# Kernel optimization log

Hardware: AMD Instinct MI355X
Metric: run time of the kernel (lower is better)

## Reference

```python
import jax, jax.numpy as jnp
import numpy as np

B, C, H, W = 16, 512, 64, 64
R = 8
CP = C // R  # inner channel dim C' = 64


def setup_inputs() -> dict:
    key = jax.random.key(0)
    ks = jax.random.split(key, 10)
    s_in = 1.0 / np.sqrt(C)
    s_cp = 1.0 / np.sqrt(CP)
    return {
        "x": jax.random.normal(ks[0], (B, C, H, W), dtype=jnp.float32),
        "wq": jax.random.uniform(ks[1], (CP, C), jnp.float32, -s_in, s_in),
        "bq": jax.random.uniform(ks[2], (CP,), jnp.float32, -s_in, s_in),
        "wk": jax.random.uniform(ks[3], (CP, C), jnp.float32, -s_in, s_in),
        "bk": jax.random.uniform(ks[4], (CP,), jnp.float32, -s_in, s_in),
        "wv": jax.random.uniform(ks[5], (CP, C), jnp.float32, -s_in, s_in),
        "bv": jax.random.uniform(ks[6], (CP,), jnp.float32, -s_in, s_in),
        "wo": jax.random.uniform(ks[7], (C, CP), jnp.float32, -s_cp, s_cp),
        "bo": jax.random.uniform(ks[8], (C,), jnp.float32, -s_cp, s_cp),
        # torch init is gamma=0 (output==x, zero grads to convs); use small
        # nonzero value so the reference exercises the full graph.
        "gamma": jax.random.normal(ks[9], (1,), dtype=jnp.float32) * 0.1,
    }


def reference(x, wq, bq, wk, bk, wv, bv, wo, bo, gamma):
    b, c, h, w = x.shape
    n = h * w
    xf = x.reshape(b, c, n)  # flatten spatial -> (B, C, N)
    # 1x1 convs == channel matmuls
    q = jnp.einsum("oc,bcn->bon", wq, xf) + bq[:, None]  # (B, C', N)
    k = jnp.einsum("oc,bcn->bon", wk, xf) + bk[:, None]  # (B, C', N)
    v = jnp.einsum("oc,bcn->bon", wv, xf) + bv[:, None]  # (B, C', N)
    # energy = bmm(key (B,C',N), query^T (B,N,C')) -> (B, C', C')
    energy = jnp.einsum("bin,bjn->bij", k, q)
    attention = jax.nn.softmax(energy, axis=-1)  # (B, C', C')
    out = jnp.einsum("bij,bjn->bin", attention, v)  # (B, C', N)
    out = jnp.einsum("co,bon->bcn", wo, out) + bo[:, None]  # (B, C, N)
    out = out.reshape(b, c, h, w)
    return gamma * out + x
```

## Files before the change

### kernel.cpp

```cpp
#include <hip/hip_runtime.h>


#define NN 4096
#define CIN 512
#define CPD 64

typedef short s8v __attribute__((ext_vector_type(8)));
typedef float f4v __attribute__((ext_vector_type(4)));
typedef unsigned short u16;

__device__ __forceinline__ u16 f2bf(float f) {
    union { float f; unsigned int u; } c; c.f = f;
    unsigned int r = c.u + 0x7FFFu + ((c.u >> 16) & 1u);
    return (u16)(r >> 16);
}

__global__ __launch_bounds__(256) void k_prep(
    const float* __restrict__ wq, const float* __restrict__ wk,
    const float* __restrict__ wv, const float* __restrict__ wo,
    u16* __restrict__ wqkvb, u16* __restrict__ wob)
{
    const int t = blockIdx.x * 256 + threadIdx.x;
    const int i4 = t * 4;
    const float* src; u16* dst; int off;
    if (i4 < 98304) {
        const int r = i4 >> 15;
        src = (r == 0) ? wq : (r == 1) ? wk : wv;
        off = i4 & 32767;
        dst = wqkvb + (r << 15);
    } else {
        src = wo; off = i4 - 98304; dst = wob;
    }
    float4 v = *(const float4*)(src + off);
    u16 tmp[4] = { f2bf(v.x), f2bf(v.y), f2bf(v.z), f2bf(v.w) };
    *(uint2*)(dst + off) = *(const uint2*)tmp;
}

__global__ __launch_bounds__(256) void k_xt(
    const float* __restrict__ x, u16* __restrict__ xt)
{
    const int ct = blockIdx.x, nt = blockIdx.y, b = blockIdx.z;
    const int t = threadIdx.x;
    const int c0 = ct * 64, n0 = nt * 64;
    __shared__ u16 lt[64 * 64];

    #pragma unroll
    for (int p = 0; p < 4; ++p) {
        const int c_l = p * 16 + (t >> 4);
        const int n4  = (t & 15) * 4;
        float4 v = *(const float4*)(x + ((size_t)b * CIN + c0 + c_l) * NN + n0 + n4);
        u16 tmp[4] = { f2bf(v.x), f2bf(v.y), f2bf(v.z), f2bf(v.w) };
        *(uint2*)&lt[c_l * 64 + (n4 ^ ((c_l >> 3) << 3))] = *(const uint2*)tmp;
    }
    __syncthreads();

    #pragma unroll
    for (int pp = 0; pp < 2; ++pp) {
        const int n_l = pp * 32 + (t >> 3);
        const int cg  = (t & 7) * 8;
        const int swz = (t & 7) << 3;
        u16 tmp[8];
        #pragma unroll
        for (int i = 0; i < 8; ++i)
            tmp[i] = lt[(cg + i) * 64 + (n_l ^ swz)];
        *(uint4*)(xt + ((size_t)b * NN + n0 + n_l) * CIN + c0 + cg) =
            *(const uint4*)tmp;
    }
}

__global__ __launch_bounds__(256, 4) void k_qkv(
    const u16* __restrict__ xt, const u16* __restrict__ wqkvb,
    const float* __restrict__ bq, const float* __restrict__ bk,
    const float* __restrict__ bv,
    u16* __restrict__ q, u16* __restrict__ k, u16* __restrict__ vt)
{
    const int nb = blockIdx.x, b = blockIdx.y;
    const int t = threadIdx.x;
    const int w = t >> 6, L = t & 63, quad = L >> 4, l15 = L & 15;
    const int n0 = nb * 64;

    f4v acc[3][4];
    #pragma unroll
    for (int p = 0; p < 3; ++p)
        #pragma unroll
        for (int nn = 0; nn < 4; ++nn) acc[p][nn] = (f4v){0.f,0.f,0.f,0.f};

    const u16* xb = xt + ((size_t)b * NN + n0) * CIN;
    const u16* wb = wqkvb + (size_t)(w * 16 + l15) * CIN;

    #pragma unroll
    for (int ks = 0; ks < 16; ++ks) {
        const int c = ks * 32 + quad * 8;
        s8v bf[4], af[3];
        #pragma unroll
        for (int nn = 0; nn < 4; ++nn)
            bf[nn] = *(const s8v*)(xb + (size_t)(nn * 16 + l15) * CIN + c);
        #pragma unroll
        for (int p = 0; p < 3; ++p)
            af[p] = *(const s8v*)(wb + (size_t)p * 64 * CIN + c);
        #pragma unroll
        for (int p = 0; p < 3; ++p)
            #pragma unroll
            for (int nn = 0; nn < 4; ++nn)
                acc[p][nn] = __builtin_amdgcn_mfma_f32_16x16x32_bf16(
                    af[p], bf[nn], acc[p][nn], 0, 0, 0);
    }

    const int orow = w * 16 + quad * 4;
    {
        float4 q4 = *(const float4*)(bq + orow);
        float4 k4 = *(const float4*)(bk + orow);
        const float qb_[4] = { q4.x, q4.y, q4.z, q4.w };
        const float kb_[4] = { k4.x, k4.y, k4.z, k4.w };
        u16* qp = q + (size_t)b * CPD * NN;
        u16* kp = k + (size_t)b * CPD * NN;
        #pragma unroll
        for (int nn = 0; nn < 4; ++nn) {
            const int n = n0 + nn * 16 + l15;
            #pragma unroll
            for (int r = 0; r < 4; ++r) {
                qp[(size_t)(orow + r) * NN + n] = f2bf(acc[0][nn][r] + qb_[r]);
                kp[(size_t)(orow + r) * NN + n] = f2bf(acc[1][nn][r] + kb_[r]);
            }
        }
    }
    {
        float4 v4 = *(const float4*)(bv + orow);
        const float vb_[4] = { v4.x, v4.y, v4.z, v4.w };
        u16* vtb = vt + (size_t)b * NN * CPD;
        #pragma unroll
        for (int nn = 0; nn < 4; ++nn) {
            const int n = n0 + nn * 16 + l15;
            u16 tmp[4];
            #pragma unroll
            for (int r = 0; r < 4; ++r) tmp[r] = f2bf(acc[2][nn][r] + vb_[r]);
            *(uint2*)(vtb + (size_t)n * CPD + orow) = *(const uint2*)tmp;
        }
    }
}

__global__ __launch_bounds__(256, 4) void k_energy(
    const u16* __restrict__ q, const u16* __restrict__ k,
    float* __restrict__ epart)
{
    const int s = blockIdx.x;
    const int b = blockIdx.y;
    const int t = threadIdx.x;
    const int wv_ = t >> 6, L = t & 63, quad = L >> 4, l15 = L & 15;
    const u16* kb = k + (size_t)b * CPD * NN;
    const u16* qb = q + (size_t)b * CPD * NN;

    f4v acc[4][4];
    #pragma unroll
    for (int a = 0; a < 4; ++a)
        #pragma unroll
        for (int d = 0; d < 4; ++d) acc[a][d] = (f4v){0.f,0.f,0.f,0.f};

    const int nbase = s * 512 + wv_ * 128;
    #pragma unroll
    for (int ksl = 0; ksl < 4; ++ksl) {
        const int n = nbase + ksl * 32 + quad * 8;
        s8v af[4], bf_[4];
        #pragma unroll
        for (int it = 0; it < 4; ++it)
            af[it] = *(const s8v*)(kb + (size_t)(it * 16 + l15) * NN + n);
        #pragma unroll
        for (int jt = 0; jt < 4; ++jt)
            bf_[jt] = *(const s8v*)(qb + (size_t)(jt * 16 + l15) * NN + n);
        #pragma unroll
        for (int it = 0; it < 4; ++it)
            #pragma unroll
            for (int jt = 0; jt < 4; ++jt)
                acc[it][jt] = __builtin_amdgcn_mfma_f32_16x16x32_bf16(
                    af[it], bf_[jt], acc[it][jt], 0, 0, 0);
    }

    float* ep = epart + ((size_t)b * 32 + s * 4 + wv_) * 4096;
    #pragma unroll
    for (int it = 0; it < 4; ++it)
        #pragma unroll
        for (int jt = 0; jt < 4; ++jt)
            #pragma unroll
            for (int r = 0; r < 4; ++r)
                ep[(it * 16 + quad * 4 + r) * 64 + jt * 16 + l15] =
                    acc[it][jt][r];
}

__global__ __launch_bounds__(64) void k_softmax(
    const float* __restrict__ epart, u16* __restrict__ attn)
{
    const int i = blockIdx.x;
    const int b = blockIdx.y;
    const int j = threadIdx.x;
    float s = 0.f;
    #pragma unroll
    for (int sp = 0; sp < 32; ++sp)
        s += epart[((size_t)b * 32 + sp) * 4096 + i * 64 + j];
    float m = s;
    #pragma unroll
    for (int off = 32; off; off >>= 1) m = fmaxf(m, __shfl_xor(m, off));
    float e = __expf(s - m);
    float tot = e;
    #pragma unroll
    for (int off = 32; off; off >>= 1) tot += __shfl_xor(tot, off);
    attn[(size_t)b * 4096 + i * 64 + j] = f2bf(e / tot);
}

__global__ __launch_bounds__(256, 4) void k_avout(
    const u16* __restrict__ vt, const u16* __restrict__ attn,
    const u16* __restrict__ wob, const float* __restrict__ bo,
    const float* __restrict__ gamma, const float* __restrict__ x,
    float* __restrict__ out)
{
    const int nb = blockIdx.x, b = blockIdx.y;
    const int t = threadIdx.x;
    const int wv_ = t >> 6, L = t & 63, quad = L >> 4, l15 = L & 15;
    const int swz = (l15 & 7) * 8;

    __shared__ u16 avl[128 * 64];

    {
        const u16* ab  = attn + (size_t)b * 4096;
        const u16* vtb = vt + (size_t)b * NN * CPD;
        const int n0 = nb * 128;
        f4v acc1[4][2];
        #pragma unroll
        for (int a = 0; a < 4; ++a)
            #pragma unroll
            for (int d = 0; d < 2; ++d) acc1[a][d] = (f4v){0.f,0.f,0.f,0.f};
        #pragma unroll
        for (int ks = 0; ks < 2; ++ks) {
            const int j = ks * 32 + quad * 8;
            s8v af[4], bf_[2];
            #pragma unroll
            for (int it = 0; it < 4; ++it)
                af[it] = *(const s8v*)(ab + (size_t)(it * 16 + l15) * 64 + j);
            #pragma unroll
            for (int nn = 0; nn < 2; ++nn)
                bf_[nn] = *(const s8v*)(vtb +
                    (size_t)(n0 + wv_ * 32 + nn * 16 + l15) * CPD + j);
            #pragma unroll
            for (int it = 0; it < 4; ++it)
                #pragma unroll
                for (int nn = 0; nn < 2; ++nn)
                    acc1[it][nn] = __builtin_amdgcn_mfma_f32_16x16x32_bf16(
                        af[it], bf_[nn], acc1[it][nn], 0, 0, 0);
        }
        #pragma unroll
        for (int it = 0; it < 4; ++it)
            #pragma unroll
            for (int nn = 0; nn < 2; ++nn) {
                const int nloc = wv_ * 32 + nn * 16 + l15;
                u16 tmp[4];
                #pragma unroll
                for (int r = 0; r < 4; ++r) tmp[r] = f2bf(acc1[it][nn][r]);
                *(uint2*)&avl[nloc * 64 + ((it * 16 + quad * 4) ^ swz)] =
                    *(const uint2*)tmp;
            }
    }
    __syncthreads();

    const float g = gamma[0];
    const int n0 = nb * 128;
    for (int cb = 0; cb < 8; ++cb) {
        f4v acc2[2][4];
        #pragma unroll
        for (int a = 0; a < 2; ++a)
            #pragma unroll
            for (int d = 0; d < 4; ++d) acc2[a][d] = (f4v){0.f,0.f,0.f,0.f};
        #pragma unroll
        for (int ks = 0; ks < 2; ++ks) {
            const int i0 = ks * 32 + quad * 8;
            const int ic = i0 ^ swz;
            s8v af2[2], bf2[4];
            #pragma unroll
            for (int nt = 0; nt < 2; ++nt)
                af2[nt] = *(const s8v*)&avl[(wv_ * 32 + nt * 16 + l15) * 64 + ic];
            #pragma unroll
            for (int ct = 0; ct < 4; ++ct)
                bf2[ct] = *(const s8v*)(wob +
                    (size_t)(cb * 64 + ct * 16 + l15) * CPD + i0);
            #pragma unroll
            for (int nt = 0; nt < 2; ++nt)
                #pragma unroll
                for (int ct = 0; ct < 4; ++ct)
                    acc2[nt][ct] = __builtin_amdgcn_mfma_f32_16x16x32_bf16(
                        af2[nt], bf2[ct], acc2[nt][ct], 0, 0, 0);
        }
        #pragma unroll
        for (int nt = 0; nt < 2; ++nt)
            #pragma unroll
            for (int ct = 0; ct < 4; ++ct) {
                const int c = cb * 64 + ct * 16 + l15;
                const float bs = bo[c];
                const int nbase = n0 + wv_ * 32 + nt * 16 + quad * 4;
                const size_t idx = ((size_t)b * CIN + c) * NN + nbase;
                float4 xr = *(const float4*)(x + idx);
                float4 r4;
                r4.x = g * (acc2[nt][ct][0] + bs) + xr.x;
                r4.y = g * (acc2[nt][ct][1] + bs) + xr.y;
                r4.z = g * (acc2[nt][ct][2] + bs) + xr.z;
                r4.w = g * (acc2[nt][ct][3] + bs) + xr.w;
                *(float4*)(out + idx) = r4;
            }
    }
}

extern "C" void kernel_launch(void* const* d_in, const int* in_sizes, int n_in,
                              void* d_out, int out_size, void* d_ws, size_t ws_size,
                              hipStream_t stream) {
    const float* x  = (const float*)d_in[0];
    const float* wq = (const float*)d_in[1];
    const float* bq = (const float*)d_in[2];
    const float* wk = (const float*)d_in[3];
    const float* bk = (const float*)d_in[4];
    const float* wv = (const float*)d_in[5];
    const float* bv = (const float*)d_in[6];
    const float* wo = (const float*)d_in[7];
    const float* bo = (const float*)d_in[8];
    const float* gm = (const float*)d_in[9];
    float* out = (float*)d_out;

    char* wsb = (char*)d_ws;
    u16*   xt    = (u16*)wsb;
    u16*   q     = (u16*)(wsb + 67108864);
    u16*   k     = (u16*)(wsb + 75497472);
    u16*   vt    = (u16*)(wsb + 83886080);
    float* epart = (float*)(wsb + 92274688);
    u16*   attn  = (u16*)(wsb + 100663296);
    u16*   wqkvb = (u16*)(wsb + 100794368);
    u16*   wob   = (u16*)(wsb + 100990976);

    k_prep<<<128, 256, 0, stream>>>(wq, wk, wv, wo, wqkvb, wob);
    k_xt<<<dim3(8, 64, 16), 256, 0, stream>>>(x, xt);
    k_qkv<<<dim3(64, 16), 256, 0, stream>>>(xt, wqkvb, bq, bk, bv, q, k, vt);
    k_energy<<<dim3(8, 16), 256, 0, stream>>>(q, k, epart);
    k_softmax<<<dim3(64, 16), 64, 0, stream>>>(epart, attn);
    k_avout<<<dim3(32, 16), 256, 0, stream>>>(vt, attn, wob, bo, gm, x, out);
}
```

Before: 387.1 us.

## Fuse x transpose/bf16 convert into QKV GEMM and halve avout tile

Drops the separate k_xt kernel, which wrote a transposed bf16 copy of x to workspace. k_qkv now reads fp32 x directly, converts it to bf16 and stages 64-channel chunks in double-buffered, XOR-swizzled shared memory, prefetching the next chunk into registers while doing MFMAs on the current one. This removes a full write and re-read of the 64 MB intermediate, at the cost of strided fp32 global loads and more LDS traffic inside the GEMM. Separately, k_avout is retiled to 64 columns per block with twice as many blocks, which gives more parallelism but reloads wo more often.

Measured after the change: 346.6 us. -10.5%, faster.

```diff
diff --git a/kernel.cpp b/kernel.cpp
--- a/kernel.cpp
+++ b/kernel.cpp
@@ -14,6 +14,8 @@
     unsigned int r = c.u + 0x7FFFu + ((c.u >> 16) & 1u);
     return (u16)(r >> 16);
 }
+
+union PK { uint2 u[2]; s8v v; };
 
 __global__ __launch_bounds__(256) void k_prep(
     const float* __restrict__ wq, const float* __restrict__ wk,
@@ -36,40 +38,8 @@
     *(uint2*)(dst + off) = *(const uint2*)tmp;
 }
 
-__global__ __launch_bounds__(256) void k_xt(
-    const float* __restrict__ x, u16* __restrict__ xt)
-{
-    const int ct = blockIdx.x, nt = blockIdx.y, b = blockIdx.z;
-    const int t = threadIdx.x;
-    const int c0 = ct * 64, n0 = nt * 64;
-    __shared__ u16 lt[64 * 64];
-
-    #pragma unroll
-    for (int p = 0; p < 4; ++p) {
-        const int c_l = p * 16 + (t >> 4);
-        const int n4  = (t & 15) * 4;
-        float4 v = *(const float4*)(x + ((size_t)b * CIN + c0 + c_l) * NN + n0 + n4);
-        u16 tmp[4] = { f2bf(v.x), f2bf(v.y), f2bf(v.z), f2bf(v.w) };
-        *(uint2*)&lt[c_l * 64 + (n4 ^ ((c_l >> 3) << 3))] = *(const uint2*)tmp;
-    }
-    __syncthreads();
-
-    #pragma unroll
-    for (int pp = 0; pp < 2; ++pp) {
-        const int n_l = pp * 32 + (t >> 3);
-        const int cg  = (t & 7) * 8;
-        const int swz = (t & 7) << 3;
-        u16 tmp[8];
-        #pragma unroll
-        for (int i = 0; i < 8; ++i)
-            tmp[i] = lt[(cg + i) * 64 + (n_l ^ swz)];
-        *(uint4*)(xt + ((size_t)b * NN + n0 + n_l) * CIN + c0 + cg) =
-            *(const uint4*)tmp;
-    }
-}
-
 __global__ __launch_bounds__(256, 4) void k_qkv(
-    const u16* __restrict__ xt, const u16* __restrict__ wqkvb,
+    const float* __restrict__ x, const u16* __restrict__ wqkvb,
     const float* __restrict__ bq, const float* __restrict__ bk,
     const float* __restrict__ bv,
     u16* __restrict__ q, u16* __restrict__ k, u16* __restrict__ vt)
@@ -79,31 +49,78 @@
     const int w = t >> 6, L = t & 63, quad = L >> 4, l15 = L & 15;
     const int n0 = nb * 64;
 
+    __shared__ u16 xs[2][64 * 64];
+
+    const int nl = t & 63, c4b = t >> 6;
+    const float* xp = x + (size_t)b * CIN * NN + n0 + nl;
+
     f4v acc[3][4];
     #pragma unroll
     for (int p = 0; p < 3; ++p)
         #pragma unroll
         for (int nn = 0; nn < 4; ++nn) acc[p][nn] = (f4v){0.f,0.f,0.f,0.f};
 
-    const u16* xb = xt + ((size_t)b * NN + n0) * CIN;
     const u16* wb = wqkvb + (size_t)(w * 16 + l15) * CIN;
 
-    #pragma unroll
-    for (int ks = 0; ks < 16; ++ks) {
-        const int c = ks * 32 + quad * 8;
-        s8v bf[4], af[3];
-        #pragma unroll
-        for (int nn = 0; nn < 4; ++nn)
-            bf[nn] = *(const s8v*)(xb + (size_t)(nn * 16 + l15) * CIN + c);
-        #pragma unroll
-        for (int p = 0; p < 3; ++p)
-            af[p] = *(const s8v*)(wb + (size_t)p * 64 * CIN + c);
-        #pragma unroll
-        for (int p = 0; p < 3; ++p)
-            #pragma unroll
-            for (int nn = 0; nn < 4; ++nn)
-                acc[p][nn] = __builtin_amdgcn_mfma_f32_16x16x32_bf16(
-                    af[p], bf[nn], acc[p][nn], 0, 0, 0);
+    float xr[16];
+    #pragma unroll
+    for (int i = 0; i < 4; ++i)
+        #pragma unroll
+        for (int j = 0; j < 4; ++j)
+            xr[i * 4 + j] = xp[(size_t)((c4b + 4 * i) * 4 + j) * NN];
+    #pragma unroll
+    for (int i = 0; i < 4; ++i) {
+        u16 t4[4];
+        #pragma unroll
+        for (int j = 0; j < 4; ++j) t4[j] = f2bf(xr[i * 4 + j]);
+        const int slot = (c4b + 4 * i) ^ (nl & 15);
+        *(uint2*)&xs[0][nl * 64 + slot * 4] = *(const uint2*)t4;
+    }
+    __syncthreads();
+
+    for (int cc = 0; cc < 8; ++cc) {
+        const int buf = cc & 1;
+        if (cc < 7) {
+            const int c0n = (cc + 1) * 64;
+            #pragma unroll
+            for (int i = 0; i < 4; ++i)
+                #pragma unroll
+                for (int j = 0; j < 4; ++j)
+                    xr[i * 4 + j] = xp[(size_t)(c0n + (c4b + 4 * i) * 4 + j) * NN];
+        }
+        #pragma unroll
+        for (int ks2 = 0; ks2 < 2; ++ks2) {
+            s8v bf[4];
+            #pragma unroll
+            for (int nn = 0; nn < 4; ++nn) {
+                const int row = nn * 16 + l15;
+                const int sb = ks2 * 8 + quad * 2;
+                PK p_;
+                p_.u[0] = *(const uint2*)&xs[buf][row * 64 + ((sb ^ l15) * 4)];
+                p_.u[1] = *(const uint2*)&xs[buf][row * 64 + (((sb + 1) ^ l15) * 4)];
+                bf[nn] = p_.v;
+            }
+            const int cgl = cc * 64 + ks2 * 32 + quad * 8;
+            #pragma unroll
+            for (int p = 0; p < 3; ++p) {
+                s8v af = *(const s8v*)(wb + (size_t)p * 64 * CIN + cgl);
+                #pragma unroll
+                for (int nn = 0; nn < 4; ++nn)
+                    acc[p][nn] = __builtin_amdgcn_mfma_f32_16x16x32_bf16(
+                        af, bf[nn], acc[p][nn], 0, 0, 0);
+            }
+        }
+        if (cc < 7) {
+            #pragma unroll
+            for (int i = 0; i < 4; ++i) {
+                u16 t4[4];
+                #pragma unroll
+                for (int j = 0; j < 4; ++j) t4[j] = f2bf(xr[i * 4 + j]);
+                const int slot = (c4b + 4 * i) ^ (nl & 15);
+                *(uint2*)&xs[buf ^ 1][nl * 64 + slot * 4] = *(const uint2*)t4;
+            }
+        }
+        __syncthreads();
     }
 
     const int orow = w * 16 + quad * 4;
@@ -215,94 +232,74 @@
     const int nb = blockIdx.x, b = blockIdx.y;
     const int t = threadIdx.x;
     const int wv_ = t >> 6, L = t & 63, quad = L >> 4, l15 = L & 15;
-    const int swz = (l15 & 7) * 8;
-
-    __shared__ u16 avl[128 * 64];
+    const int n0 = nb * 64;
+
+    __shared__ u16 avl[64 * 64];
 
     {
         const u16* ab  = attn + (size_t)b * 4096;
         const u16* vtb = vt + (size_t)b * NN * CPD;
-        const int n0 = nb * 128;
-        f4v acc1[4][2];
-        #pragma unroll
-        for (int a = 0; a < 4; ++a)
-            #pragma unroll
-            for (int d = 0; d < 2; ++d) acc1[a][d] = (f4v){0.f,0.f,0.f,0.f};
+        f4v acc1[4];
+        #pragma unroll
+        for (int a = 0; a < 4; ++a) acc1[a] = (f4v){0.f,0.f,0.f,0.f};
+        const int nloc = wv_ * 16 + l15;
         #pragma unroll
         for (int ks = 0; ks < 2; ++ks) {
             const int j = ks * 32 + quad * 8;
-            s8v af[4], bf_[2];
-            #pragma unroll
-            for (int it = 0; it < 4; ++it)
-                af[it] = *(const s8v*)(ab + (size_t)(it * 16 + l15) * 64 + j);
-            #pragma unroll
-            for (int nn = 0; nn < 2; ++nn)
-                bf_[nn] = *(const s8v*)(vtb +
-                    (size_t)(n0 + wv_ * 32 + nn * 16 + l15) * CPD + j);
-            #pragma unroll
-            for (int it = 0; it < 4; ++it)
-                #pragma unroll
-                for (int nn = 0; nn < 2; ++nn)
-                    acc1[it][nn] = __builtin_amdgcn_mfma_f32_16x16x32_bf16(
-                        af[it], bf_[nn], acc1[it][nn], 0, 0, 0);
-        }
-        #pragma unroll
-        for (int it = 0; it < 4; ++it)
-            #pragma unroll
-            for (int nn = 0; nn < 2; ++nn) {
-                const int nloc = wv_ * 32 + nn * 16 + l15;
-                u16 tmp[4];
-                #pragma unroll
-                for (int r = 0; r < 4; ++r) tmp[r] = f2bf(acc1[it][nn][r]);
-                *(uint2*)&avl[nloc * 64 + ((it * 16 + quad * 4) ^ swz)] =
-                    *(const uint2*)tmp;
-            }
+            s8v bfv = *(const s8v*)(vtb + (size_t)(n0 + nloc) * CPD + j);
+            #pragma unroll
+            for (int it = 0; it < 4; ++it) {
+                s8v af = *(const s8v*)(ab + (size_t)(it * 16 + l15) * 64 + j);
+                acc1[it] = __builtin_amdgcn_mfma_f32_16x16x32_bf16(
+                    af, bfv, acc1[it], 0, 0, 0);
+            }
+        }
+        #pragma unroll
+        for (int it = 0; it < 4; ++it) {
+            u16 t4[4];
+            #pragma unroll
+            for (int r = 0; r < 4; ++r) t4[r] = f2bf(acc1[it][r]);
+            const int slot = (it * 4 + quad) ^ l15;
+            *(uint2*)&avl[nloc * 64 + slot * 4] = *(const uint2*)t4;
+        }
     }
     __syncthreads();
 
     const float g = gamma[0];
-    const int n0 = nb * 128;
     for (int cb = 0; cb < 8; ++cb) {
-        f4v acc2[2][4];
-        #pragma unroll
-        for (int a = 0; a < 2; ++a)
-            #pragma unroll
-            for (int d = 0; d < 4; ++d) acc2[a][d] = (f4v){0.f,0.f,0.f,0.f};
+        f4v acc2[4];
+        #pragma unroll
+        for (int a = 0; a < 4; ++a) acc2[a] = (f4v){0.f,0.f,0.f,0.f};
         #pragma unroll
         for (int ks = 0; ks < 2; ++ks) {
+            const int sb = ks * 8 + quad * 2;
+            PK p_;
+            p_.u[0] = *(const uint2*)&avl[(wv_ * 16 + l15) * 64 + ((sb ^ l15) * 4)];
+            p_.u[1] = *(const uint2*)&avl[(wv_ * 16 + l15) * 64 + (((sb + 1) ^ l15) * 4)];
+            const s8v af2 = p_.v;
             const int i0 = ks * 32 + quad * 8;
-            const int ic = i0 ^ swz;
-            s8v af2[2], bf2[4];
-            #pragma unroll
-            for (int nt = 0; nt < 2; ++nt)
-                af2[nt] = *(const s8v*)&avl[(wv_ * 32 + nt * 16 + l15) * 64 + ic];
-            #pragma unroll
-            for (int ct = 0; ct < 4; ++ct)
-                bf2[ct] = *(const s8v*)(wob +
+            #pragma unroll
+            for (int ct = 0; ct < 4; ++ct) {
+                s8v bf2 = *(const s8v*)(wob +
                     (size_t)(cb * 64 + ct * 16 + l15) * CPD + i0);
-            #pragma unroll
-            for (int nt = 0; nt < 2; ++nt)
-                #pragma unroll
-                for (int ct = 0; ct < 4; ++ct)
-                    acc2[nt][ct] = __builtin_amdgcn_mfma_f32_16x16x32_bf16(
-                        af2[nt], bf2[ct], acc2[nt][ct], 0, 0, 0);
-        }
-        #pragma unroll
-        for (int nt = 0; nt < 2; ++nt)
-            #pragma unroll
-            for (int ct = 0; ct < 4; ++ct) {
-                const int c = cb * 64 + ct * 16 + l15;
-                const float bs = bo[c];
-                const int nbase = n0 + wv_ * 32 + nt * 16 + quad * 4;
-                const size_t idx = ((size_t)b * CIN + c) * NN + nbase;
-                float4 xr = *(const float4*)(x + idx);
-                float4 r4;
-                r4.x = g * (acc2[nt][ct][0] + bs) + xr.x;
-                r4.y = g * (acc2[nt][ct][1] + bs) + xr.y;
-                r4.z = g * (acc2[nt][ct][2] + bs) + xr.z;
-                r4.w = g * (acc2[nt][ct][3] + bs) + xr.w;
-                *(float4*)(out + idx) = r4;
-            }
+                acc2[ct] = __builtin_amdgcn_mfma_f32_16x16x32_bf16(
+                    af2, bf2, acc2[ct], 0, 0, 0);
+            }
+        }
+        #pragma unroll
+        for (int ct = 0; ct < 4; ++ct) {
+            const int c = cb * 64 + ct * 16 + l15;
+            const float bs = bo[c];
+            const int nb4 = n0 + wv_ * 16 + quad * 4;
+            const size_t idx = ((size_t)b * CIN + c) * NN + nb4;
+            float4 xr = *(const float4*)(x + idx);
+            float4 r4;
+            r4.x = g * (acc2[ct][0] + bs) + xr.x;
+            r4.y = g * (acc2[ct][1] + bs) + xr.y;
+            r4.z = g * (acc2[ct][2] + bs) + xr.z;
+            r4.w = g * (acc2[ct][3] + bs) + xr.w;
+            *(float4*)(out + idx) = r4;
+        }
     }
 }
 
@@ -322,19 +319,17 @@
     float* out = (float*)d_out;
 
     char* wsb = (char*)d_ws;
-    u16*   xt    = (u16*)wsb;
-    u16*   q     = (u16*)(wsb + 67108864);
-    u16*   k     = (u16*)(wsb + 75497472);
-    u16*   vt    = (u16*)(wsb + 83886080);
-    float* epart = (float*)(wsb + 92274688);
-    u16*   attn  = (u16*)(wsb + 100663296);
-    u16*   wqkvb = (u16*)(wsb + 100794368);
-    u16*   wob   = (u16*)(wsb + 100990976);
+    u16*   q     = (u16*)wsb;
+    u16*   k     = (u16*)(wsb + 8388608);
+    u16*   vt    = (u16*)(wsb + 16777216);
+    float* epart = (float*)(wsb + 25165824);
+    u16*   attn  = (u16*)(wsb + 33554432);
+    u16*   wqkvb = (u16*)(wsb + 33685504);
+    u16*   wob   = (u16*)(wsb + 33882112);
 
     k_prep<<<128, 256, 0, stream>>>(wq, wk, wv, wo, wqkvb, wob);
-    k_xt<<<dim3(8, 64, 16), 256, 0, stream>>>(x, xt);
-    k_qkv<<<dim3(64, 16), 256, 0, stream>>>(xt, wqkvb, bq, bk, bv, q, k, vt);
+    k_qkv<<<dim3(64, 16), 256, 0, stream>>>(x, wqkvb, bq, bk, bv, q, k, vt);
     k_energy<<<dim3(8, 16), 256, 0, stream>>>(q, k, epart);
     k_softmax<<<dim3(64, 16), 64, 0, stream>>>(epart, attn);
-    k_avout<<<dim3(32, 16), 256, 0, stream>>>(vt, attn, wob, bo, gm, x, out);
-}
+    k_avout<<<dim3(64, 16), 256, 0, stream>>>(vt, attn, wob, bo, gm, x, out);
+}
```
